# Performance work log

Hardware: AMD Instinct MI355X
Metric: run time of the kernel (lower is better)

The kernel has to match this reference:

```python
import jax, jax.numpy as jnp
import numpy as np

MEMORY_SLOTS = 256
MEMORY_TOPK = 8
RETRIEVAL_WEIGHT = 0.5


def setup_inputs() -> dict:
    key = jax.random.key(0)
    ks = jax.random.split(key, 5)
    B, T, C = 8, 2048, 1024
    scale = 1.0 / np.sqrt(C)
    return {
        "x": jax.random.normal(ks[0], (B, T, C), dtype=jnp.float32),
        "Wq": jax.random.normal(ks[1], (C, C), dtype=jnp.float32) * scale,
        "Wk": jax.random.normal(ks[2], (C, C), dtype=jnp.float32) * scale,
        "Wv": jax.random.normal(ks[3], (C, C), dtype=jnp.float32) * scale,
        "Wp": jax.random.normal(ks[4], (C, C), dtype=jnp.float32) * scale,
    }


def reference(x, Wq, Wk, Wv, Wp):
    B, T, C = x.shape
    num_slots = min(T, MEMORY_SLOTS)
    topk = min(num_slots, MEMORY_TOPK)
    # adaptive_avg_pool1d with T divisible by num_slots == mean over equal chunks
    slots = x.reshape(B, num_slots, T // num_slots, C).mean(axis=2)  # [B,S,C]
    # Linear layers (torch: x @ W.T, no bias)
    q = jnp.einsum("btc,dc->btd", x, Wq)        # [B,T,C]
    k = jnp.einsum("bsc,dc->bsd", slots, Wk)    # [B,S,C]
    v = jnp.einsum("bsc,dc->bsd", slots, Wv)    # [B,S,C]
    scores = jnp.einsum("btd,bsd->bts", q, k) * (1.0 / jnp.sqrt(jnp.float32(C)))
    topk_scores, topk_indices = jax.lax.top_k(scores, topk)  # [B,T,K]
    topk_weights = jax.nn.softmax(topk_scores, axis=-1)       # [B,T,K]
    # gather selected value rows: [B,T,K,C]
    retrieved = jnp.take_along_axis(v[:, None, :, :], topk_indices[..., None], axis=2)
    retrieved = jnp.einsum("btkc,btk->btc", retrieved, topk_weights)
    out = jnp.einsum("btc,dc->btd", retrieved, Wp) * RETRIEVAL_WEIGHT
    return out
```

## Files before the change

### kernel.cpp

```cpp
#include <hip/hip_runtime.h>
#include <cstdint>
#include <cstddef>

#define Tt 2048
#define Cc 1024
#define Ss 256

using short8 = __attribute__((ext_vector_type(8))) short;
using f32x4  = __attribute__((ext_vector_type(4))) float;
typedef const __attribute__((address_space(1))) void* as1_cvp;
typedef __attribute__((address_space(3))) void* as3_vp;

__device__ __forceinline__ unsigned short f2bf(float f) {
  unsigned int u = __float_as_uint(f);
  u += 0x7fffu + ((u >> 16) & 1u);
  return (unsigned short)(u >> 16);
}
__device__ __forceinline__ float bf2f(unsigned short h) {
  return __uint_as_float(((unsigned)h) << 16);
}
__device__ __forceinline__ void split3(float v, unsigned short& h, unsigned short& m, unsigned short& l) {
  h = f2bf(v);
  float r = v - bf2f(h);
  m = f2bf(r);
  l = f2bf(r - bf2f(m));
}

__device__ __forceinline__ int sw32(int row, int q) {
  return row * 32 + ((q ^ ((row >> 1) & 3)) << 3);
}

__global__ __launch_bounds__(256) void poolsplit_k(const float* __restrict__ x, unsigned short* __restrict__ sp) {
  const long PS2 = 2048l * 1024;
  const int sli = blockIdx.x;
  const int c = threadIdx.x << 2;
  const float* src = x + (size_t)sli * 8 * Cc + c;
  float a[4] = {0.f, 0.f, 0.f, 0.f};
#pragma unroll
  for (int j = 0; j < 8; j++) {
    float4 v = *(const float4*)(src + (size_t)j * Cc);
    a[0] += v.x; a[1] += v.y; a[2] += v.z; a[3] += v.w;
  }
  unsigned short h[4], m[4], l[4];
#pragma unroll
  for (int e = 0; e < 4; e++) split3(a[e] * 0.125f, h[e], m[e], l[e]);
  size_t o = (size_t)sli * Cc + c;
  *(uint2*)&sp[o]           = uint2{(unsigned)h[0] | ((unsigned)h[1] << 16), (unsigned)h[2] | ((unsigned)h[3] << 16)};
  *(uint2*)&sp[o + PS2]     = uint2{(unsigned)m[0] | ((unsigned)m[1] << 16), (unsigned)m[2] | ((unsigned)m[3] << 16)};
  *(uint2*)&sp[o + 2 * PS2] = uint2{(unsigned)l[0] | ((unsigned)l[1] << 16), (unsigned)l[2] | ((unsigned)l[3] << 16)};
}

__global__ __launch_bounds__(256) void split_t_k(const float* __restrict__ src, unsigned short* __restrict__ dst,
                                                 long pstride, int npl) {
  __shared__ unsigned short th[64][68], tm[64][68], tl[64][68];
  const int r0 = blockIdx.y << 6, c0 = blockIdx.x << 6;
  const int tid = threadIdx.x;
#pragma unroll
  for (int p = 0; p < 4; p++) {
    int r = (p << 4) + (tid >> 4);
    int c = (tid & 15) << 2;
    float4 v = *(const float4*)&src[(size_t)(r0 + r) * Cc + c0 + c];
    unsigned short h, m, l;
    split3(v.x, h, m, l); th[c + 0][r] = h; tm[c + 0][r] = m; tl[c + 0][r] = l;
    split3(v.y, h, m, l); th[c + 1][r] = h; tm[c + 1][r] = m; tl[c + 1][r] = l;
    split3(v.z, h, m, l); th[c + 2][r] = h; tm[c + 2][r] = m; tl[c + 2][r] = l;
    split3(v.w, h, m, l); th[c + 3][r] = h; tm[c + 3][r] = m; tl[c + 3][r] = l;
  }
  __syncthreads();
#pragma unroll
  for (int p = 0; p < 4; p++) {
    int r = (p << 4) + (tid >> 4);
    int c = (tid & 15) << 2;
    size_t o = (size_t)(c0 + r) * Cc + r0 + c;
    *(uint2*)&dst[o] = uint2{(unsigned)th[r][c] | ((unsigned)th[r][c+1] << 16),
                             (unsigned)th[r][c+2] | ((unsigned)th[r][c+3] << 16)};
    *(uint2*)&dst[o + pstride] = uint2{(unsigned)tm[r][c] | ((unsigned)tm[r][c+1] << 16),
                                       (unsigned)tm[r][c+2] | ((unsigned)tm[r][c+3] << 16)};
    if (npl == 3)
      *(uint2*)&dst[o + 2 * pstride] = uint2{(unsigned)tl[r][c] | ((unsigned)tl[r][c+1] << 16),
                                             (unsigned)tl[r][c+2] | ((unsigned)tl[r][c+3] << 16)};
  }
}

__global__ __launch_bounds__(256) void split_k(const float* __restrict__ src, unsigned short* __restrict__ dst,
                                               long pstride, int npl) {
  int id = blockIdx.x * 256 + threadIdx.x;
  int c = id << 2;
  float4 v = *(const float4*)&src[c];
  unsigned short h[4], m[4], l[4];
  split3(v.x, h[0], m[0], l[0]); split3(v.y, h[1], m[1], l[1]);
  split3(v.z, h[2], m[2], l[2]); split3(v.w, h[3], m[3], l[3]);
  *(uint2*)&dst[c] = uint2{(unsigned)h[0] | ((unsigned)h[1] << 16), (unsigned)h[2] | ((unsigned)h[3] << 16)};
  *(uint2*)&dst[c + pstride] = uint2{(unsigned)m[0] | ((unsigned)m[1] << 16), (unsigned)m[2] | ((unsigned)m[3] << 16)};
  if (npl == 3)
    *(uint2*)&dst[c + 2 * pstride] = uint2{(unsigned)l[0] | ((unsigned)l[1] << 16), (unsigned)l[2] | ((unsigned)l[3] << 16)};
}

template<int NT, int SPLIT_OUT>
__device__ __forceinline__ void gemm3_body(const unsigned short* __restrict__ Ap, long apl,
                                           const unsigned short* __restrict__ Bp, long bpl,
                                           float* __restrict__ C,
                                           unsigned short* __restrict__ Cs, long cpl,
                                           float scale) {
  constexpr int NPL = (NT == 6) ? 3 : 2;
  __shared__ unsigned short LDS[2 * NPL * 2048];
  const int tid = threadIdx.x, lane = tid & 63, wid = tid >> 6;
  const int m0 = blockIdx.y << 6, n0 = blockIdx.x << 6;

  const unsigned short* sp[2 * NPL];
  as3_vp dst[2 * NPL];
#pragma unroll
  for (int i = 0; i < 2 * NPL; i++) {
    int s = wid * 2 * NPL + i;
    int tile = s >> 2;
    int ci = ((s & 3) << 6) | lane;
    int row = ci >> 2;
    int q = (ci & 3) ^ ((row >> 1) & 3);
    int isB = tile >= NPL;
    int pl = isB ? tile - NPL : tile;
    const unsigned short* base = isB ? (Bp + (size_t)pl * bpl) : (Ap + (size_t)pl * apl);
    int r0 = isB ? n0 : m0;
    sp[i] = base + (size_t)(r0 + row) * Cc + (q << 3);
    dst[i] = (as3_vp)(LDS + tile * 2048 + ((s & 3) << 9));
  }

  const int wm = (wid >> 1) << 5, wn = (wid & 1) << 5;
  const int lm = lane & 15, lq = lane >> 4;
  constexpr int PA[6] = {0, 0, 1, 0, 2, 1};
  constexpr int PB[6] = {0, 1, 0, 2, 0, 1};
  const f32x4 zero = {0.f, 0.f, 0.f, 0.f};
  f32x4 acc[2][2] = {{zero, zero}, {zero, zero}};

  for (int k0 = 0; k0 < Cc; k0 += 32) {
    __syncthreads();
#pragma unroll
    for (int i = 0; i < 2 * NPL; i++) {
      __builtin_amdgcn_global_load_lds((as1_cvp)sp[i], dst[i], 16, 0, 0);
      sp[i] += 32;
    }
    __syncthreads();
    short8 af[2][NPL], bf[2][NPL];
#pragma unroll
    for (int i = 0; i < 2; i++)
#pragma unroll
      for (int p = 0; p < NPL; p++) {
        af[i][p] = *(const short8*)&LDS[p * 2048 + sw32(wm + (i << 4) + lm, lq)];
        bf[i][p] = *(const short8*)&LDS[(NPL + p) * 2048 + sw32(wn + (i << 4) + lm, lq)];
      }
#pragma unroll
    for (int i = 0; i < 2; i++)
#pragma unroll
      for (int j = 0; j < 2; j++)
#pragma unroll
        for (int t = 0; t < NT; t++)
          acc[i][j] = __builtin_amdgcn_mfma_f32_16x16x32_bf16(af[i][PA[t]], bf[j][PB[t]], acc[i][j], 0, 0, 0);
  }
#pragma unroll
  for (int i = 0; i < 2; i++)
#pragma unroll
    for (int j = 0; j < 2; j++)
#pragma unroll
      for (int r = 0; r < 4; r++) {
        int gr = m0 + wm + (i << 4) + (lq << 2) + r;
        int gc = n0 + wn + (j << 4) + lm;
        size_t o = (size_t)gr * Cc + gc;
        float v = acc[i][j][r] * scale;
        if (SPLIT_OUT) {
          unsigned short h = f2bf(v);
          float rr = v - bf2f(h);
          unsigned short mm2 = f2bf(rr);
          Cs[o] = h;
          Cs[o + cpl] = mm2;
          if (NPL == 3) Cs[o + 2 * (size_t)cpl] = f2bf(rr - bf2f(mm2));
        } else {
          C[o] = v;
        }
      }
}

__global__ __launch_bounds__(256) void gemm3_61_k(const unsigned short* __restrict__ Ap, long apl,
                                                  const unsigned short* __restrict__ Bp, long bpl,
                                                  unsigned short* __restrict__ Cs, long cpl, float scale) {
  gemm3_body<6, 1>(Ap, apl, Bp, bpl, nullptr, Cs, cpl, scale);
}
__global__ __launch_bounds__(256) void gemm3_31_k(const unsigned short* __restrict__ Ap, long apl,
                                                  const unsigned short* __restrict__ Bp, long bpl,
                                                  unsigned short* __restrict__ Cs, long cpl, float scale) {
  gemm3_body<3, 1>(Ap, apl, Bp, bpl, nullptr, Cs, cpl, scale);
}
__global__ __launch_bounds__(256) void gemm3_30_k(const unsigned short* __restrict__ Ap, long apl,
                                                  const unsigned short* __restrict__ Bp, long bpl,
                                                  float* __restrict__ C, float scale) {
  gemm3_body<3, 0>(Ap, apl, Bp, bpl, C, nullptr, 0, scale);
}

__global__ __launch_bounds__(512) void scores_topk_k(const float* __restrict__ x,
                                                     const unsigned short* __restrict__ kqp,
                                                     float* __restrict__ topw, int* __restrict__ topi) {
  __shared__ __align__(16) char smem[71168];
  float* xf = (float*)smem;
  unsigned short* lds16 = (unsigned short*)smem;
  float* sc = (float*)smem;

  const int tid = threadIdx.x, lane = tid & 63, wid = tid >> 6;
  const int tt = blockIdx.x, b = blockIdx.y;
  const float* xb = x + ((size_t)b * Tt + (size_t)tt * 64) * Cc;

  const char* srcs[7]; int step[7]; as3_vp ldst[7];
#pragma unroll
  for (int i = 0; i < 7; i++) {
    int s = wid * 7 + i;
    if (s < 8) {
      int ci = (s << 6) | lane;
      int row = ci >> 3, off = (ci & 7) << 2;
      srcs[i] = (const char*)(xb + (size_t)row * Cc + off);
      step[i] = 128;
      ldst[i] = (as3_vp)(smem + s * 1024);
    } else {
      int p = (s - 8) >> 4;
      int sub = (s - 8) & 15;
      int ci = (sub << 6) | lane;
      int row = ci >> 2;
      int q = (ci & 3) ^ ((row >> 1) & 3);
      const unsigned short* kb = kqp + (size_t)p * (2048l * 1024) + (size_t)b * Ss * Cc;
      srcs[i] = (const char*)(kb + (size_t)row * Cc + (q << 3));
      step[i] = 64;
      ldst[i] = (as3_vp)(smem + 8192 + p * 16384 + (sub << 10));
    }
  }

  const int wm = (wid & 1) << 5;
  const int wn = (wid >> 1) << 6;
  const int lm = lane & 15, lq = lane >> 4;
  const int spr = tid >> 3, spk = (tid & 7) << 2;
  const int XS = 28672;

  constexpr int PA[6] = {0, 0, 1, 0, 2, 1};
  constexpr int PB[6] = {0, 1, 0, 2, 0, 1};
  const f32x4 zero = {0.f, 0.f, 0.f, 0.f};
  f32x4 acc[2][4];
#pragma unroll
  for (int i = 0; i < 2; i++)
#pragma unroll
    for (int j = 0; j < 4; j++) acc[i][j] = zero;

  for (int ks = 0; ks < 32; ks++) {
    __syncthreads();
#pragma unroll
    for (int i = 0; i < 7; i++) {
      __builtin_amdgcn_global_load_lds((as1_cvp)srcs[i], ldst[i], 16, 0, 0);
      srcs[i] += step[i];
    }
    __syncthreads();
    {
      float4 v = *(const float4*)(xf + (tid << 2));
      unsigned short h[4], m[4], l[4];
      split3(v.x, h[0], m[0], l[0]); split3(v.y, h[1], m[1], l[1]);
      split3(v.z, h[2], m[2], l[2]); split3(v.w, h[3], m[3], l[3]);
      int o = XS + spr * 36 + spk;
      *(uint2*)&lds16[o]        = uint2{(unsigned)h[0] | ((unsigned)h[1] << 16), (unsigned)h[2] | ((unsigned)h[3] << 16)};
      *(uint2*)&lds16[o + 2304] = uint2{(unsigned)m[0] | ((unsigned)m[1] << 16), (unsigned)m[2] | ((unsigned)m[3] << 16)};
      *(uint2*)&lds16[o + 4608] = uint2{(unsigned)l[0] | ((unsigned)l[1] << 16), (unsigned)l[2] | ((unsigned)l[3] << 16)};
    }
    __syncthreads();
    short8 afr[2][3], bfr[4][3];
#pragma unroll
    for (int i = 0; i < 2; i++)
#pragma unroll
      for (int p = 0; p < 3; p++)
        afr[i][p] = *(const short8*)&lds16[XS + p * 2304 + (wm + (i << 4) + lm) * 36 + (lq << 3)];
#pragma unroll
    for (int j = 0; j < 4; j++) {
      int br = wn + (j << 4) + lm;
      int bo = (br << 5) + ((lq ^ ((br >> 1) & 3)) << 3);
#pragma unroll
      for (int p = 0; p < 3; p++)
        bfr[j][p] = *(const short8*)&lds16[4096 + p * 8192 + bo];
    }
#pragma unroll
    for (int i = 0; i < 2; i++)
#pragma unroll
      for (int j = 0; j < 4; j++)
#pragma unroll
        for (int t = 0; t < 6; t++)
          acc[i][j] = __builtin_amdgcn_mfma_f32_16x16x32_bf16(afr[i][PA[t]], bfr[j][PB[t]], acc[i][j], 0, 0, 0);
  }

  __syncthreads();
#pragma unroll
  for (int i = 0; i < 2; i++)
#pragma unroll
    for (int j = 0; j < 4; j++)
#pragma unroll
      for (int r = 0; r < 4; r++)
        sc[(wm + (i << 4) + (lq << 2) + r) * 260 + wn + (j << 4) + lm] = acc[i][j][r] * 0.03125f;
  __syncthreads();

  for (int r2 = 0; r2 < 8; r2++) {
    int row = (wid << 3) + r2;
    float4 v = *(const float4*)(sc + row * 260 + (lane << 2));
    float cand[4] = {v.x, v.y, v.z, v.w};
    float topv[8]; int tops[8];
#pragma unroll
    for (int k = 0; k < 8; k++) {
      float bv = -1e30f; int bs = 1 << 20;
#pragma unroll
      for (int e = 0; e < 4; e++) {
        int s = (lane << 2) + e;
        if (cand[e] > bv || (cand[e] == bv && s < bs)) { bv = cand[e]; bs = s; }
      }
#pragma unroll
      for (int m = 32; m >= 1; m >>= 1) {
        float ov = __shfl_xor(bv, m, 64);
        int   os = __shfl_xor(bs, m, 64);
        if (ov > bv || (ov == bv && os < bs)) { bv = ov; bs = os; }
      }
      topv[k] = bv; tops[k] = bs;
      if ((bs >> 2) == lane) cand[bs & 3] = -1e30f;
    }
    float mx = topv[0];
    float sum = 0.f;
#pragma unroll
    for (int k = 0; k < 8; k++) sum += expf(topv[k] - mx);
    if (lane < 8) {
      float myv = topv[0]; int myi = tops[0];
#pragma unroll
      for (int k = 1; k < 8; k++) if (lane == k) { myv = topv[k]; myi = tops[k]; }
      size_t trow = (size_t)b * Tt + (size_t)tt * 64 + row;
      topw[trow * 8 + lane] = expf(myv - mx) / sum;
      topi[trow * 8 + lane] = myi;
    }
  }
}

__global__ __launch_bounds__(256) void gatherout_k(const float* __restrict__ u, const float* __restrict__ topw,
                                                   const int* __restrict__ topi, float* __restrict__ out) {
  __shared__ float w[8];
  __shared__ int  id8[8];
  const int row = blockIdx.x;
  const int b = row >> 11;
  if (threadIdx.x < 8) {
    w[threadIdx.x]   = topw[(size_t)row * 8 + threadIdx.x];
    id8[threadIdx.x] = topi[(size_t)row * 8 + threadIdx.x];
  }
  __syncthreads();
  int c = threadIdx.x << 2;
  float ax = 0.f, ay = 0.f, az = 0.f, aw = 0.f;
#pragma unroll
  for (int j = 0; j < 8; j++) {
    const float4 vv = *(const float4*)&u[((size_t)(b << 8) + id8[j]) * Cc + c];
    float wj = w[j];
    ax = fmaf(wj, vv.x, ax); ay = fmaf(wj, vv.y, ay);
    az = fmaf(wj, vv.z, az); aw = fmaf(wj, vv.w, aw);
  }
  *(float4*)&out[(size_t)row * Cc + c] = make_float4(ax * 0.5f, ay * 0.5f, az * 0.5f, aw * 0.5f);
}

extern "C" void kernel_launch(void* const* d_in, const int* in_sizes, int n_in,
                              void* d_out, int out_size, void* d_ws, size_t ws_size,
                              hipStream_t stream) {
  (void)in_sizes; (void)n_in; (void)out_size; (void)ws_size;
  const float* x  = (const float*)d_in[0];
  const float* Wq = (const float*)d_in[1];
  const float* Wk = (const float*)d_in[2];
  const float* Wv = (const float*)d_in[3];
  const float* Wp = (const float*)d_in[4];
  float* out = (float*)d_out;

  char* ws = (char*)d_ws;
  const size_t MB = 1ull << 20;
  const long PS1 = 1024l * 1024;
  const long PS2 = 2048l * 1024;
  unsigned short* slotp = (unsigned short*)(ws + 0 * MB);
  unsigned short* Wqt   = (unsigned short*)(ws + 12 * MB);
  unsigned short* Wkt   = (unsigned short*)(ws + 18 * MB);
  unsigned short* Wvt   = (unsigned short*)(ws + 24 * MB);
  unsigned short* Wpp   = (unsigned short*)(ws + 28 * MB);
  unsigned short* MtT   = (unsigned short*)(ws + 32 * MB);
  unsigned short* kqp   = (unsigned short*)(ws + 38 * MB);
  unsigned short* W2p   = (unsigned short*)(ws + 50 * MB);
  float*          u     = (float*)(ws + 54 * MB);
  float*          topw  = (float*)(ws + 62 * MB);
  int*            topi  = (int*)(ws + 62 * MB + 512 * 1024);

  poolsplit_k<<<2048, 256, 0, stream>>>(x, slotp);
  split_t_k<<<dim3(16, 16), 256, 0, stream>>>(Wq, Wqt, PS1, 3);
  split_t_k<<<dim3(16, 16), 256, 0, stream>>>(Wk, Wkt, PS1, 3);
  split_t_k<<<dim3(16, 16), 256, 0, stream>>>(Wv, Wvt, PS1, 2);
  split_k<<<1024, 256, 0, stream>>>(Wp, Wpp, PS1, 2);
  gemm3_61_k<<<dim3(16, 16), 256, 0, stream>>>(Wqt, PS1, Wkt, PS1, MtT, PS1, 1.0f);
  gemm3_61_k<<<dim3(16, 32), 256, 0, stream>>>(slotp, PS2, MtT, PS1, kqp, PS2, 1.0f);
  gemm3_31_k<<<dim3(16, 16), 256, 0, stream>>>(Wpp, PS1, Wvt, PS1, W2p, PS1, 1.0f);
  gemm3_30_k<<<dim3(16, 32), 256, 0, stream>>>(slotp, PS2, W2p, PS1, u, 1.0f);
  scores_topk_k<<<dim3(32, 8), 512, 0, stream>>>(x, kqp, topw, topi);
  gatherout_k<<<16384, 256, 0, stream>>>(u, topw, topi, out);
}
```

Measured before the change: 417.4 us.

## Double-buffer LDS tiles in GEMM and scores kernels to overlap loads with MFMA

Both the generic split-bf16 GEMM body and the scores/top-k kernel now keep two LDS buffers. The next K-slice is prefetched with global_load_lds while MFMAs run on the current slice, which cuts the per-iteration sync barriers from two or three to one. In the scores kernel, x is now loaded into registers and split into bf16 planes after the MFMAs rather than staged through LDS, and block indexing is remapped so batch varies fastest across blocks. LDS use rises to about 123KB per block in the scores kernel, and the one-barrier scheme depends on the async LDS writes being complete by the time the barrier passes.

After: 380.2 us. -8.9%, faster.

```diff
diff --git a/kernel.cpp b/kernel.cpp
--- a/kernel.cpp
+++ b/kernel.cpp
@@ -103,12 +103,13 @@
                                            unsigned short* __restrict__ Cs, long cpl,
                                            float scale) {
   constexpr int NPL = (NT == 6) ? 3 : 2;
-  __shared__ unsigned short LDS[2 * NPL * 2048];
+  constexpr int BUFS = 2 * NPL * 2048;
+  __shared__ unsigned short LDS[2 * BUFS];
   const int tid = threadIdx.x, lane = tid & 63, wid = tid >> 6;
   const int m0 = blockIdx.y << 6, n0 = blockIdx.x << 6;
 
   const unsigned short* sp[2 * NPL];
-  as3_vp dst[2 * NPL];
+  int dof[2 * NPL];
 #pragma unroll
   for (int i = 0; i < 2 * NPL; i++) {
     int s = wid * 2 * NPL + i;
@@ -121,7 +122,7 @@
     const unsigned short* base = isB ? (Bp + (size_t)pl * bpl) : (Ap + (size_t)pl * apl);
     int r0 = isB ? n0 : m0;
     sp[i] = base + (size_t)(r0 + row) * Cc + (q << 3);
-    dst[i] = (as3_vp)(LDS + tile * 2048 + ((s & 3) << 9));
+    dof[i] = (tile * 2048 + ((s & 3) << 9)) * 2;
   }
 
   const int wm = (wid >> 1) << 5, wn = (wid & 1) << 5;
@@ -131,21 +132,31 @@
   const f32x4 zero = {0.f, 0.f, 0.f, 0.f};
   f32x4 acc[2][2] = {{zero, zero}, {zero, zero}};
 
+#pragma unroll
+  for (int i = 0; i < 2 * NPL; i++) {
+    __builtin_amdgcn_global_load_lds((as1_cvp)sp[i], (as3_vp)((char*)LDS + dof[i]), 16, 0, 0);
+    sp[i] += 32;
+  }
+  __syncthreads();
+
+  int cur = 0;
   for (int k0 = 0; k0 < Cc; k0 += 32) {
-    __syncthreads();
-#pragma unroll
-    for (int i = 0; i < 2 * NPL; i++) {
-      __builtin_amdgcn_global_load_lds((as1_cvp)sp[i], dst[i], 16, 0, 0);
-      sp[i] += 32;
-    }
-    __syncthreads();
+    if (k0 + 32 < Cc) {
+      const int nb = (cur ^ 1) * (BUFS * 2);
+#pragma unroll
+      for (int i = 0; i < 2 * NPL; i++) {
+        __builtin_amdgcn_global_load_lds((as1_cvp)sp[i], (as3_vp)((char*)LDS + nb + dof[i]), 16, 0, 0);
+        sp[i] += 32;
+      }
+    }
+    const int cb = cur * BUFS;
     short8 af[2][NPL], bf[2][NPL];
 #pragma unroll
     for (int i = 0; i < 2; i++)
 #pragma unroll
       for (int p = 0; p < NPL; p++) {
-        af[i][p] = *(const short8*)&LDS[p * 2048 + sw32(wm + (i << 4) + lm, lq)];
-        bf[i][p] = *(const short8*)&LDS[(NPL + p) * 2048 + sw32(wn + (i << 4) + lm, lq)];
+        af[i][p] = *(const short8*)&LDS[cb + p * 2048 + sw32(wm + (i << 4) + lm, lq)];
+        bf[i][p] = *(const short8*)&LDS[cb + (NPL + p) * 2048 + sw32(wn + (i << 4) + lm, lq)];
       }
 #pragma unroll
     for (int i = 0; i < 2; i++)
@@ -154,6 +165,8 @@
 #pragma unroll
         for (int t = 0; t < NT; t++)
           acc[i][j] = __builtin_amdgcn_mfma_f32_16x16x32_bf16(af[i][PA[t]], bf[j][PB[t]], acc[i][j], 0, 0, 0);
+    __syncthreads();
+    cur ^= 1;
   }
 #pragma unroll
   for (int i = 0; i < 2; i++)
@@ -197,43 +210,33 @@
 __global__ __launch_bounds__(512) void scores_topk_k(const float* __restrict__ x,
                                                      const unsigned short* __restrict__ kqp,
                                                      float* __restrict__ topw, int* __restrict__ topi) {
-  __shared__ __align__(16) char smem[71168];
-  float* xf = (float*)smem;
+  __shared__ __align__(16) char smem[125952];
   unsigned short* lds16 = (unsigned short*)smem;
   float* sc = (float*)smem;
 
   const int tid = threadIdx.x, lane = tid & 63, wid = tid >> 6;
-  const int tt = blockIdx.x, b = blockIdx.y;
-  const float* xb = x + ((size_t)b * Tt + (size_t)tt * 64) * Cc;
-
-  const char* srcs[7]; int step[7]; as3_vp ldst[7];
-#pragma unroll
-  for (int i = 0; i < 7; i++) {
-    int s = wid * 7 + i;
-    if (s < 8) {
-      int ci = (s << 6) | lane;
-      int row = ci >> 3, off = (ci & 7) << 2;
-      srcs[i] = (const char*)(xb + (size_t)row * Cc + off);
-      step[i] = 128;
-      ldst[i] = (as3_vp)(smem + s * 1024);
-    } else {
-      int p = (s - 8) >> 4;
-      int sub = (s - 8) & 15;
-      int ci = (sub << 6) | lane;
-      int row = ci >> 2;
-      int q = (ci & 3) ^ ((row >> 1) & 3);
-      const unsigned short* kb = kqp + (size_t)p * (2048l * 1024) + (size_t)b * Ss * Cc;
-      srcs[i] = (const char*)(kb + (size_t)row * Cc + (q << 3));
-      step[i] = 64;
-      ldst[i] = (as3_vp)(smem + 8192 + p * 16384 + (sub << 10));
-    }
-  }
+  const int bid = blockIdx.x;
+  const int b = bid & 7, tt = bid >> 3;
+
+  const char* ksrc[6];
+  int kdst[6];
+#pragma unroll
+  for (int i = 0; i < 6; i++) {
+    int s = wid * 6 + i;
+    int p = s >> 4, sub = s & 15;
+    int ci = (sub << 6) | lane;
+    int row = ci >> 2;
+    int q = (ci & 3) ^ ((row >> 1) & 3);
+    ksrc[i] = (const char*)(kqp + (size_t)p * (2048l * 1024) + ((size_t)b * Ss + row) * Cc + (q << 3));
+    kdst[i] = p * 16384 + sub * 1024;
+  }
+  const int spr = tid >> 3, spk = (tid & 7) << 2;
+  const float* xsrc = x + ((size_t)b * Tt + (size_t)tt * 64 + spr) * Cc + spk;
 
   const int wm = (wid & 1) << 5;
   const int wn = (wid >> 1) << 6;
   const int lm = lane & 15, lq = lane >> 4;
-  const int spr = tid >> 3, spk = (tid & 7) << 2;
-  const int XS = 28672;
+  const int XP = 49152;
 
   constexpr int PA[6] = {0, 0, 1, 0, 2, 1};
   constexpr int PB[6] = {0, 1, 0, 2, 0, 1};
@@ -244,49 +247,71 @@
 #pragma unroll
     for (int j = 0; j < 4; j++) acc[i][j] = zero;
 
+  {
+    float4 xv = *(const float4*)xsrc; xsrc += 32;
+#pragma unroll
+    for (int i = 0; i < 6; i++) {
+      __builtin_amdgcn_global_load_lds((as1_cvp)ksrc[i], (as3_vp)(smem + kdst[i]), 16, 0, 0);
+      ksrc[i] += 64;
+    }
+    unsigned short h[4], m[4], l[4];
+    split3(xv.x, h[0], m[0], l[0]); split3(xv.y, h[1], m[1], l[1]);
+    split3(xv.z, h[2], m[2], l[2]); split3(xv.w, h[3], m[3], l[3]);
+    int o = XP + spr * 36 + spk;
+    *(uint2*)&lds16[o]        = uint2{(unsigned)h[0] | ((unsigned)h[1] << 16), (unsigned)h[2] | ((unsigned)h[3] << 16)};
+    *(uint2*)&lds16[o + 2304] = uint2{(unsigned)m[0] | ((unsigned)m[1] << 16), (unsigned)m[2] | ((unsigned)m[3] << 16)};
+    *(uint2*)&lds16[o + 4608] = uint2{(unsigned)l[0] | ((unsigned)l[1] << 16), (unsigned)l[2] | ((unsigned)l[3] << 16)};
+  }
+  __syncthreads();
+
+  int cur = 0;
   for (int ks = 0; ks < 32; ks++) {
-    __syncthreads();
-#pragma unroll
-    for (int i = 0; i < 7; i++) {
-      __builtin_amdgcn_global_load_lds((as1_cvp)srcs[i], ldst[i], 16, 0, 0);
-      srcs[i] += step[i];
-    }
-    __syncthreads();
-    {
-      float4 v = *(const float4*)(xf + (tid << 2));
+    const int nb = cur ^ 1;
+    float4 xv2;
+    if (ks < 31) {
+      xv2 = *(const float4*)xsrc; xsrc += 32;
+#pragma unroll
+      for (int i = 0; i < 6; i++) {
+        __builtin_amdgcn_global_load_lds((as1_cvp)ksrc[i], (as3_vp)(smem + nb * 49152 + kdst[i]), 16, 0, 0);
+        ksrc[i] += 64;
+      }
+    }
+    const int xb = XP + cur * 6912;
+    const int kb = cur * 24576;
+    short8 afr[2][3], bfr[4][3];
+#pragma unroll
+    for (int i = 0; i < 2; i++)
+#pragma unroll
+      for (int p = 0; p < 3; p++)
+        afr[i][p] = *(const short8*)&lds16[xb + p * 2304 + (wm + (i << 4) + lm) * 36 + (lq << 3)];
+#pragma unroll
+    for (int j = 0; j < 4; j++) {
+      int br = wn + (j << 4) + lm;
+      int bo = (br << 5) + ((lq ^ ((br >> 1) & 3)) << 3);
+#pragma unroll
+      for (int p = 0; p < 3; p++)
+        bfr[j][p] = *(const short8*)&lds16[kb + p * 8192 + bo];
+    }
+#pragma unroll
+    for (int i = 0; i < 2; i++)
+#pragma unroll
+      for (int j = 0; j < 4; j++)
+#pragma unroll
+        for (int t = 0; t < 6; t++)
+          acc[i][j] = __builtin_amdgcn_mfma_f32_16x16x32_bf16(afr[i][PA[t]], bfr[j][PB[t]], acc[i][j], 0, 0, 0);
+    if (ks < 31) {
       unsigned short h[4], m[4], l[4];
-      split3(v.x, h[0], m[0], l[0]); split3(v.y, h[1], m[1], l[1]);
-      split3(v.z, h[2], m[2], l[2]); split3(v.w, h[3], m[3], l[3]);
-      int o = XS + spr * 36 + spk;
+      split3(xv2.x, h[0], m[0], l[0]); split3(xv2.y, h[1], m[1], l[1]);
+      split3(xv2.z, h[2], m[2], l[2]); split3(xv2.w, h[3], m[3], l[3]);
+      int o = XP + nb * 6912 + spr * 36 + spk;
       *(uint2*)&lds16[o]        = uint2{(unsigned)h[0] | ((unsigned)h[1] << 16), (unsigned)h[2] | ((unsigned)h[3] << 16)};
       *(uint2*)&lds16[o + 2304] = uint2{(unsigned)m[0] | ((unsigned)m[1] << 16), (unsigned)m[2] | ((unsigned)m[3] << 16)};
       *(uint2*)&lds16[o + 4608] = uint2{(unsigned)l[0] | ((unsigned)l[1] << 16), (unsigned)l[2] | ((unsigned)l[3] << 16)};
     }
     __syncthreads();
-    short8 afr[2][3], bfr[4][3];
-#pragma unroll
-    for (int i = 0; i < 2; i++)
-#pragma unroll
-      for (int p = 0; p < 3; p++)
-        afr[i][p] = *(const short8*)&lds16[XS + p * 2304 + (wm + (i << 4) + lm) * 36 + (lq << 3)];
-#pragma unroll
-    for (int j = 0; j < 4; j++) {
-      int br = wn + (j << 4) + lm;
-      int bo = (br << 5) + ((lq ^ ((br >> 1) & 3)) << 3);
-#pragma unroll
-      for (int p = 0; p < 3; p++)
-        bfr[j][p] = *(const short8*)&lds16[4096 + p * 8192 + bo];
-    }
-#pragma unroll
-    for (int i = 0; i < 2; i++)
-#pragma unroll
-      for (int j = 0; j < 4; j++)
-#pragma unroll
-        for (int t = 0; t < 6; t++)
-          acc[i][j] = __builtin_amdgcn_mfma_f32_16x16x32_bf16(afr[i][PA[t]], bfr[j][PB[t]], acc[i][j], 0, 0, 0);
-  }
-
-  __syncthreads();
+    cur ^= 1;
+  }
+
 #pragma unroll
   for (int i = 0; i < 2; i++)
 #pragma unroll
@@ -392,6 +417,6 @@
   gemm3_61_k<<<dim3(16, 32), 256, 0, stream>>>(slotp, PS2, MtT, PS1, kqp, PS2, 1.0f);
   gemm3_31_k<<<dim3(16, 16), 256, 0, stream>>>(Wpp, PS1, Wvt, PS1, W2p, PS1, 1.0f);
   gemm3_30_k<<<dim3(16, 32), 256, 0, stream>>>(slotp, PS2, W2p, PS1, u, 1.0f);
-  scores_topk_k<<<dim3(32, 8), 512, 0, stream>>>(x, kqp, topw, topi);
+  scores_topk_k<<<256, 512, 0, stream>>>(x, kqp, topw, topi);
   gatherout_k<<<16384, 256, 0, stream>>>(u, topw, topi, out);
 }
```
